# Kernel optimization log

Measured on AMD Instinct MI355X. Metric: run time of the kernel, lower is better.

The kernel has to match this reference:

```python
import jax, jax.numpy as jnp
import numpy as np

S, B, F, D, DF, NH, FH = 1152, 2, 128, 1024, 2048, 8, 4
SEP = 1024
EPS = 1e-5

def ln(x, g, b):
    m = x.mean(-1, keepdims=True)
    v = ((x - m) ** 2).mean(-1, keepdims=True)
    return (x - m) * jax.lax.rsqrt(v + EPS) * g + b

def mha(q, k, v, wi, bi, wo, bo, nh):
    # torch MultiheadAttention, batch_first=False: inputs (L, N, E)
    E = q.shape[-1]
    hd = E // nh
    qh = (q @ wi[:E].T + bi[:E]).reshape(q.shape[0], -1, nh, hd)
    kh = (k @ wi[E:2 * E].T + bi[E:2 * E]).reshape(k.shape[0], -1, nh, hd)
    vh = (v @ wi[2 * E:].T + bi[2 * E:]).reshape(k.shape[0], -1, nh, hd)
    s = jnp.einsum('qnhd,knhd->nhqk', qh, kh) / jnp.sqrt(jnp.float32(hd))
    a = jax.nn.softmax(s, axis=-1)
    o = jnp.einsum('nhqk,knhd->qnhd', a, vh).reshape(q.shape[0], -1, E)
    return o @ wo.T + bo

def setup_inputs() -> dict:
    key = jax.random.key(0)
    it = iter(jax.random.split(key, 40))
    def p(shape, s=0.02):
        return jax.random.normal(next(it), shape, jnp.float32) * s
    z = lambda *sh: jnp.zeros(sh, jnp.float32)
    o = lambda *sh: jnp.ones(sh, jnp.float32)
    return dict(
        src=jax.random.normal(next(it), (S, B, F), jnp.float32),
        sep=SEP,
        sa_wi=p((3 * D, D)), sa_bi=z(3 * D), sa_wo=p((D, D)), sa_bo=z(D),
        fa_wi=p((3 * F, F)), fa_bi=z(3 * F), fa_wo=p((F, F)), fa_bo=z(F),
        pl1_w=p((F, 1)), pl1_b=z(F),
        pl2_w=p((DF, F)), pl2_b=z(DF),
        pl3_w=p((1, DF)), pl3_b=z(1),
        pl4_w=p((DF, F)), pl4_b=z(DF),
        pl5_w=p((D, DF)), pl5_b=z(D),
        pl6_w=p((DF, D)), pl6_b=z(DF),
        pl7_w=p((D, DF)), pl7_b=z(D),
        l1_w=p((DF, D)), l1_b=z(DF),
        l2_w=p((F, DF)), l2_b=z(F),
        pn1_g=o(F), pn1_b=z(F),
        pn2_g=o(D), pn2_b=z(D),
        n1_g=o(D), n1_b=z(D),
        n2_g=o(F), n2_b=z(F),
    )

def _forward(src, sa_wi, sa_bi, sa_wo, sa_bo, fa_wi, fa_bi, fa_wo, fa_bo,
             pl1_w, pl1_b, pl2_w, pl2_b, pl3_w, pl3_b, pl4_w, pl4_b,
             pl5_w, pl5_b, pl6_w, pl6_b, pl7_w, pl7_b, l1_w, l1_b, l2_w, l2_b,
             pn1_g, pn1_b, pn2_g, pn2_b, n1_g, n1_b, n2_g, n2_b, sep):
    Sn, Bn, Fn = src.shape
    relu = jax.nn.relu
    # feature-wise attention: 'b h w -> w (b h) 1'
    x = jnp.transpose(src, (2, 0, 1)).reshape(Fn, Sn * Bn, 1)
    x = x @ pl1_w.T + pl1_b                       # (F, S*B, emsize_f)
    x = mha(x, x, x, fa_wi, fa_bi, fa_wo, fa_bo, FH)
    x = relu(x @ pl2_w.T + pl2_b) @ pl3_w.T + pl3_b  # (F, S*B, 1)
    x = jnp.transpose(x.reshape(Fn, Sn, Bn), (1, 2, 0))  # 'w (b h) 1 -> b h w'
    src1 = ln(x + src, pn1_g, pn1_b)              # (S, B, F)
    src1_ = relu(src1 @ pl4_w.T + pl4_b) @ pl5_w.T + pl5_b  # (S, B, D)
    li = src1_[:sep]
    sl = mha(li, li, li, sa_wi, sa_bi, sa_wo, sa_bo, NH)
    sl = ln(sl + li, pn2_g, pn2_b)
    sl_ = relu(sl @ pl6_w.T + pl6_b) @ pl7_w.T + pl7_b
    sl_ = ln(sl_, pn2_g, pn2_b) + sl
    sr = mha(src1_[sep:], sl_, sl_, sa_wi, sa_bi, sa_wo, sa_bo, NH)
    src2 = jnp.concatenate([sl, sr], axis=0)      # (S, B, D)
    so = ln(src2 + src1_, n1_g, n1_b)
    ff = relu(so @ l1_w.T + l1_b) @ l2_w.T + l2_b  # (S, B, F)
    return ln(src1 + ff, n2_g, n2_b)

def reference(src, sa_wi, sa_bi, sa_wo, sa_bo, fa_wi, fa_bi, fa_wo, fa_bo,
              pl1_w, pl1_b, pl2_w, pl2_b, pl3_w, pl3_b, pl4_w, pl4_b,
              pl5_w, pl5_b, pl6_w, pl6_b, pl7_w, pl7_b, l1_w, l1_b, l2_w, l2_b,
              pn1_g, pn1_b, pn2_g, pn2_b, n1_g, n1_b, n2_g, n2_b, sep):
    return _forward(src, sa_wi, sa_bi, sa_wo, sa_bo, fa_wi, fa_bi, fa_wo, fa_bo,
                    pl1_w, pl1_b, pl2_w, pl2_b, pl3_w, pl3_b, pl4_w, pl4_b,
                    pl5_w, pl5_b, pl6_w, pl6_b, pl7_w, pl7_b, l1_w, l1_b,
                    l2_w, l2_b, pn1_g, pn1_b, pn2_g, pn2_b, n1_g, n1_b,
                    n2_g, n2_b, sep)
```

## Files before the change

kernel.cpp:

```cpp
#include <hip/hip_runtime.h>

using s16x8 = __attribute__((ext_vector_type(8))) short;
using f32x4 = __attribute__((ext_vector_type(4))) float;
using f32x2 = __attribute__((ext_vector_type(2))) float;
typedef unsigned short ushort_t;

__device__ __forceinline__ unsigned short f2bf(float f) {
    union { float f; unsigned u; } v; v.f = f;
    unsigned u = v.u + 0x7FFFu + ((v.u >> 16) & 1u);
    return (unsigned short)(u >> 16);
}
__device__ __forceinline__ float bf2f(unsigned short h) {
    union { unsigned u; float f; } v; v.u = ((unsigned)h) << 16;
    return v.f;
}

__device__ __forceinline__ float block_reduce(float v, int op, float* lds) {
    const int lane = threadIdx.x & 63;
    const int w    = threadIdx.x >> 6;
    const int nw   = blockDim.x >> 6;
#pragma unroll
    for (int off = 32; off > 0; off >>= 1) {
        float o = __shfl_down(v, off, 64);
        v = op ? fmaxf(v, o) : (v + o);
    }
    __syncthreads();
    if (lane == 0) lds[w] = v;
    __syncthreads();
    float r = lds[0];
    for (int i = 1; i < nw; i++) r = op ? fmaxf(r, lds[i]) : (r + lds[i]);
    return r;
}

__device__ __forceinline__ void load_lds16(const void* g, void* l) {
    __builtin_amdgcn_global_load_lds(
        (const __attribute__((address_space(1))) unsigned int*)g,
        (__attribute__((address_space(3))) unsigned int*)l, 16, 0, 0);
}

struct CvtArgs { const float* src[8]; ushort_t* dst[8]; int end[8]; };

__global__ __launch_bounds__(256)
void cvt_all(CvtArgs a)
{
    int i = blockIdx.x * 256 + threadIdx.x;
    int j = 0;
    while (j < 8 && i >= a.end[j]) j++;
    if (j >= 8) return;
    int li = i - (j ? a.end[j - 1] : 0);
    float4 v = *(const float4*)&a.src[j][(size_t)li * 4];
    ushort_t u[4] = { f2bf(v.x), f2bf(v.y), f2bf(v.z), f2bf(v.w) };
    *(uint2*)&a.dst[j][(size_t)li * 4] = *(uint2*)u;
}

template<bool RELU, bool SPLITK>
__global__ __launch_bounds__(256, 2)
void gemm_bf16(const ushort_t* __restrict__ A, const ushort_t* __restrict__ B,
               const float* __restrict__ bias, ushort_t* __restrict__ C,
               float* __restrict__ Cp, long pstride, int ksplen, int zmod,
               int M, int N, int K, int lda, int ldb, int ldc,
               long sAz, long sBz, long sCz, long sA2, long sB2, long sC2,
               int zshift, float alpha)
{
    __shared__ ushort_t As[128 * 32];
    __shared__ ushort_t Bs[128 * 32];

    const int tid = threadIdx.x;
    int zz = blockIdx.z;
    int ks = 0, z = zz;
    if (SPLITK) { ks = zz / zmod; z = zz - ks * zmod; }
    const int z1  = z & ((1 << zshift) - 1);
    const int z2  = z >> zshift;
    const int m0  = blockIdx.x * 128;
    const int n0  = blockIdx.y * 128;

    const ushort_t* Ab = A + (size_t)z1 * sAz + (size_t)z2 * sA2 + (size_t)m0 * lda;
    const ushort_t* Bb = B + (size_t)z1 * sBz + (size_t)z2 * sB2 + (size_t)n0 * ldb;

    const int wave = tid >> 6, lane = tid & 63;
    const int wm = (wave & 1) * 64, wn = (wave >> 1) * 64;
    const int mi = lane & 15, quad = lane >> 4;

    f32x4 acc[4][4];
#pragma unroll
    for (int i = 0; i < 4; i++)
#pragma unroll
        for (int j = 0; j < 4; j++) acc[i][j] = (f32x4)0.f;

    const int r_0 = tid >> 2,           g_0 = (tid & 3) ^ ((r_0 >> 1) & 3);
    const int r_1 = (tid + 256) >> 2,   g_1 = (tid & 3) ^ ((r_1 >> 1) & 3);

    const int kbeg = SPLITK ? ks * ksplen : 0;
    const int kend = SPLITK ? kbeg + ksplen : K;

    for (int k0 = kbeg; k0 < kend; k0 += 32) {
        load_lds16(Ab + (size_t)r_0 * lda + k0 + g_0 * 8, &As[tid * 8]);
        load_lds16(Ab + (size_t)r_1 * lda + k0 + g_1 * 8, &As[(tid + 256) * 8]);
        load_lds16(Bb + (size_t)r_0 * ldb + k0 + g_0 * 8, &Bs[tid * 8]);
        load_lds16(Bb + (size_t)r_1 * ldb + k0 + g_1 * 8, &Bs[(tid + 256) * 8]);
        __syncthreads();

        s16x8 af[4], bfr[4];
#pragma unroll
        for (int t = 0; t < 4; t++) {
            int r = wm + t * 16 + mi;
            af[t] = *(const s16x8*)&As[r * 32 + ((quad ^ ((r >> 1) & 3)) * 8)];
        }
#pragma unroll
        for (int t = 0; t < 4; t++) {
            int r = wn + t * 16 + mi;
            bfr[t] = *(const s16x8*)&Bs[r * 32 + ((quad ^ ((r >> 1) & 3)) * 8)];
        }
#pragma unroll
        for (int tm = 0; tm < 4; tm++)
#pragma unroll
            for (int tn = 0; tn < 4; tn++)
                acc[tm][tn] = __builtin_amdgcn_mfma_f32_16x16x32_bf16(af[tm], bfr[tn], acc[tm][tn], 0, 0, 0);
        __syncthreads();
    }

    if (SPLITK) {
        float* Cf = Cp + (size_t)ks * pstride + (size_t)z1 * sCz + (size_t)z2 * sC2;
#pragma unroll
        for (int tn = 0; tn < 4; tn++) {
            int col = n0 + wn + tn * 16 + mi;
#pragma unroll
            for (int tm = 0; tm < 4; tm++)
#pragma unroll
                for (int r = 0; r < 4; r++) {
                    int row = m0 + wm + tm * 16 + quad * 4 + r;
                    Cf[(size_t)row * ldc + col] = acc[tm][tn][r] * alpha;
                }
        }
    } else {
#pragma unroll
        for (int tn = 0; tn < 4; tn++) {
            int col = n0 + wn + tn * 16 + mi;
            float bv = bias ? bias[col] : 0.f;
#pragma unroll
            for (int tm = 0; tm < 4; tm++) {
#pragma unroll
                for (int r = 0; r < 4; r++) {
                    int row = m0 + wm + tm * 16 + quad * 4 + r;
                    float v = acc[tm][tn][r] * alpha + bv;
                    if (RELU) v = fmaxf(v, 0.f);
                    C[(size_t)z1 * sCz + (size_t)z2 * sC2 + (size_t)row * ldc + col] = f2bf(v);
                }
            }
        }
    }
}

template<bool RELU>
__global__ __launch_bounds__(256)
void sum_cvt(const float* __restrict__ parts, long pstride, int P,
             const float* __restrict__ bias, int ldc,
             ushort_t* __restrict__ out, int total4)
{
    int i = blockIdx.x * 256 + threadIdx.x;
    if (i >= total4) return;
    size_t idx = (size_t)i * 4;
    float4 s = *(const float4*)&parts[idx];
    for (int p = 1; p < P; p++) {
        float4 v = *(const float4*)&parts[(size_t)p * pstride + idx];
        s.x += v.x; s.y += v.y; s.z += v.z; s.w += v.w;
    }
    if (bias) {
        int col = (int)(idx % (size_t)ldc);
        s.x += bias[col]; s.y += bias[col + 1]; s.z += bias[col + 2]; s.w += bias[col + 3];
    }
    if (RELU) {
        s.x = fmaxf(s.x, 0.f); s.y = fmaxf(s.y, 0.f);
        s.z = fmaxf(s.z, 0.f); s.w = fmaxf(s.w, 0.f);
    }
    ushort_t u[4] = { f2bf(s.x), f2bf(s.y), f2bf(s.z), f2bf(s.w) };
    *(uint2*)&out[idx] = *(uint2*)u;
}

__global__ __launch_bounds__(128)
void ln_part(const float* __restrict__ parts, long pstride, int P,
             const float* __restrict__ bias, const ushort_t* __restrict__ resid,
             const float* __restrict__ g, const float* __restrict__ beta,
             float* __restrict__ out)
{
    __shared__ float red[4];
    const int r = blockIdx.x, c = threadIdx.x;
    float x = bias[c] + bf2f(resid[r * 128 + c]);
    for (int p = 0; p < P; p++) x += parts[(size_t)p * pstride + (size_t)r * 128 + c];
    float s  = block_reduce(x, 0, red);
    float ss = block_reduce(x * x, 0, red);
    float mean = s * (1.f / 128.f);
    float var  = ss * (1.f / 128.f) - mean * mean;
    float inv  = rsqrtf(var + 1e-5f);
    out[(size_t)r * 128 + c] = (x - mean) * inv * g[c] + beta[c];
}

__global__ __launch_bounds__(256)
void transp128(const ushort_t* __restrict__ in, ushort_t* __restrict__ out,
               int ldin, long inz1, long inz2, long outz)
{
    __shared__ ushort_t T[64][136];
    const int z = blockIdx.z, z1 = z & 7, z2 = z >> 3;
    const int n0 = blockIdx.x * 64;
    const ushort_t* ip = in + (size_t)z1 * inz1 + (size_t)z2 * inz2;
    const int rr = threadIdx.x >> 2, cg = (threadIdx.x & 3) * 32;
#pragma unroll
    for (int c = 0; c < 4; c++) {
        s16x8 v = *(const s16x8*)(ip + (size_t)(n0 + rr) * ldin + cg + c * 8);
        *(s16x8*)&T[rr][cg + c * 8] = v;
    }
    __syncthreads();
    const int d = threadIdx.x >> 1, j0 = (threadIdx.x & 1) * 32;
    ushort_t* op = out + (size_t)z * outz + (size_t)d * 1024 + n0 + j0;
#pragma unroll
    for (int c = 0; c < 4; c++) {
        s16x8 v;
#pragma unroll
        for (int j = 0; j < 8; j++) v[j] = (short)T[j0 + c * 8 + j][d];
        *(s16x8*)(op + c * 8) = v;
    }
}

__global__ void precomp1(const float* __restrict__ fa_wi, const float* __restrict__ fa_bi,
                         const float* __restrict__ pl1_w, const float* __restrict__ pl1_b,
                         float* __restrict__ consts)
{
    int j = threadIdx.x;
    if (j < 384) {
        float u = 0.f, v = 0.f;
        for (int k = 0; k < 128; k++) {
            float w = fa_wi[j * 128 + k];
            u = fmaf(w, pl1_w[k], u);
            v = fmaf(w, pl1_b[k], v);
        }
        consts[j]       = u;
        consts[512 + j] = v + fa_bi[j];
    }
}

__global__ void precomp2(const float* __restrict__ fa_wo, const float* __restrict__ fa_bo,
                         float* __restrict__ consts)
{
    int tid = threadIdx.x;
    const float* u = consts;
    const float* v = consts + 512;
    if (tid < 16) {
        int h = tid >> 2, w = tid & 3;
        const float* ql = (w < 2) ? u : v;
        const float* kr = ((w & 1) == 0) ? u : v;
        float acc = 0.f;
        for (int d = 0; d < 32; d++) acc += ql[h * 32 + d] * kr[128 + h * 32 + d];
        consts[1024 + tid] = acc * 0.17677669529663687f;
    }
#pragma unroll
    for (int h = 0; h < 4; h++) {
        float acc = 0.f;
        for (int d = 0; d < 32; d++)
            acc = fmaf(fa_wo[tid * 128 + h * 32 + d], u[256 + h * 32 + d], acc);
        consts[1088 + h * 128 + tid] = acc;
    }
    float c0 = fa_bo[tid];
    for (int idx = 0; idx < 128; idx++)
        c0 = fmaf(fa_wo[tid * 128 + idx], v[256 + idx], c0);
    consts[1600 + tid] = c0;
}

__global__ void precomp3(const float* __restrict__ pl2_w, const float* __restrict__ pl2_b,
                         const float* __restrict__ consts, ushort_t* __restrict__ Gb)
{
    int m = blockIdx.x * 256 + threadIdx.x;
    const float* wv = consts + 1088;
    const float* c0 = consts + 1600;
    float a0 = 0.f, ah[4] = {0.f, 0.f, 0.f, 0.f};
    for (int j = 0; j < 128; j++) {
        float w = pl2_w[m * 128 + j];
        ah[0] = fmaf(w, wv[0 * 128 + j], ah[0]);
        ah[1] = fmaf(w, wv[1 * 128 + j], ah[1]);
        ah[2] = fmaf(w, wv[2 * 128 + j], ah[2]);
        ah[3] = fmaf(w, wv[3 * 128 + j], ah[3]);
        a0    = fmaf(w, c0[j], a0);
    }
    ushort_t row[8];
#pragma unroll
    for (int h = 0; h < 4; h++) row[h] = f2bf(ah[h]);
    row[4] = f2bf(a0 + pl2_b[m]);
    row[5] = row[6] = row[7] = 0;
    *(uint4*)&Gb[m * 8] = *(uint4*)row;
}

__global__ __launch_bounds__(512, 6)
void feat_mlp_ln(const float* __restrict__ src, const float* __restrict__ consts,
                 const ushort_t* __restrict__ Gb, const float* __restrict__ pl3_w,
                 const float* __restrict__ pl3_b, const float* __restrict__ pn1_g,
                 const float* __restrict__ pn1_b, ushort_t* __restrict__ src1)
{
    __shared__ ushort_t Gs[2048 * 8];
    __shared__ float    wlds[2048];
    __shared__ ushort_t Ts[128 * 8];
    __shared__ float    sv[128];
    __shared__ float    ypart[4][128];
    __shared__ float    red[8];

    const int n   = blockIdx.x;
    const int tid = threadIdx.x;
    const int f   = tid & 127;
    const int h   = tid >> 7;
    const bool act = (tid < 128);

#pragma unroll
    for (int p = 0; p < 4; p++) {
        int ci = tid + p * 512;
        load_lds16(Gb + (size_t)ci * 8, &Gs[ci * 8]);
    }
    load_lds16(pl3_w + tid * 4, &wlds[tid * 4]);
    if (act) sv[f] = src[n * 128 + f];
    __syncthreads();

    const float si = sv[f];
    float S1 = block_reduce(act ? si : 0.f, 0, red);
    float S2 = block_reduce(act ? si * si : 0.f, 0, red);
    float S3 = block_reduce(act ? si * si * si : 0.f, 0, red);
    float S4 = block_reduce(act ? si * si * si * si : 0.f, 0, red);
    float amax = block_reduce(act ? fabsf(si) : 0.f, 1, red);

    const float p_ = consts[1024 + h * 4 + 0] * si + consts[1024 + h * 4 + 2];
    float pmax = block_reduce(fabsf(p_), 1, red);

    float tt;
    if (pmax * amax < 0.25f) {
        float num = fmaf(p_, fmaf(p_, fmaf(p_, S4 * (1.f / 6.f), 0.5f * S3), S2), S1);
        float den = fmaf(p_, fmaf(p_, fmaf(p_, S3 * (1.f / 6.f), 0.5f * S2), S1), 128.f);
        tt = num / den;
    } else {
        float smax = block_reduce(act ? si : -3.4e38f, 1, red);
        float smin = -block_reduce(act ? -si : -3.4e38f, 1, red);
        float m = fmaxf(p_ * smax, p_ * smin);
        float l = 0.f, t = 0.f;
        for (int j = 0; j < 128; j++) {
            float e = __expf(fmaf(p_, sv[j], -m));
            l += e; t = fmaf(e, sv[j], t);
        }
        tt = t / l;
    }

    Ts[f * 8 + h] = f2bf(tt);
    if (act) {
        Ts[f * 8 + 4] = 0x3F80;
        Ts[f * 8 + 5] = 0; Ts[f * 8 + 6] = 0; Ts[f * 8 + 7] = 0;
    }
    __syncthreads();

    const int wave = tid >> 6, lane = tid & 63;
    const int wm = (wave & 1) * 64;
    const int mq = wave >> 1;
    const int mi = lane & 15, quad = lane >> 4;

    s16x8 af[4];
#pragma unroll
    for (int t = 0; t < 4; t++) {
        s16x8 v = *(const s16x8*)&Ts[(wm + t * 16 + mi) * 8];
        af[t] = (quad == 0) ? v : (s16x8)0;
    }

    f32x2 partial2[4][2];
#pragma unroll
    for (int i = 0; i < 4; i++) { partial2[i][0] = (f32x2)0.f; partial2[i][1] = (f32x2)0.f; }
    const f32x2 zero2 = (f32x2)0.f;

#pragma unroll 4
    for (int mt = 0; mt < 32; mt++) {
        const int m0 = mq * 512 + mt * 16;
        s16x8 bfr = *(const s16x8*)&Gs[(m0 + mi) * 8];
        float w = wlds[m0 + mi];
        f32x2 w2 = { w, w };
        f32x4 acc[4];
#pragma unroll
        for (int tm = 0; tm < 4; tm++)
            acc[tm] = __builtin_amdgcn_mfma_f32_16x16x32_bf16(af[tm], bfr, (f32x4)0.f, 0, 0, 0);
#pragma unroll
        for (int tm = 0; tm < 4; tm++) {
            f32x2* pa = (f32x2*)&acc[tm];
#pragma unroll
            for (int i = 0; i < 2; i++) {
                f32x2 r = __builtin_elementwise_max(pa[i], zero2);
                partial2[tm][i] = r * w2 + partial2[tm][i];
            }
        }
    }

#pragma unroll
    for (int tm = 0; tm < 4; tm++)
#pragma unroll
        for (int r = 0; r < 4; r++) {
            float v = partial2[tm][r >> 1][r & 1];
            v += __shfl_xor(v, 8);
            v += __shfl_xor(v, 4);
            v += __shfl_xor(v, 2);
            v += __shfl_xor(v, 1);
            if (mi == 0) ypart[mq][wm + tm * 16 + quad * 4 + r] = v;
        }
    __syncthreads();

    float yv = 0.f;
    if (act)
        yv = ypart[0][f] + ypart[1][f] + ypart[2][f] + ypart[3][f] + pl3_b[0] + sv[f];
    float s  = block_reduce(yv, 0, red);
    float ss = block_reduce(yv * yv, 0, red);
    float mean = s * (1.f / 128.f);
    float var  = ss * (1.f / 128.f) - mean * mean;
    float inv  = rsqrtf(var + 1e-5f);
    if (act)
        src1[n * 128 + f] = f2bf((yv - mean) * inv * pn1_g[f] + pn1_b[f]);
}

template<bool OUTF32>
__global__ void ln_bf16(const ushort_t* __restrict__ a, const ushort_t* __restrict__ b,
                        const ushort_t* __restrict__ post, const float* __restrict__ g,
                        const float* __restrict__ beta, void* __restrict__ out, int D)
{
    __shared__ float red[4];
    const size_t row = blockIdx.x;
    const int tid = threadIdx.x;
    const int nit = D / blockDim.x;
    const ushort_t* ap = a + row * D;
    const ushort_t* bp = b ? b + row * D : nullptr;
    float xr[4];
    float s = 0.f, ss = 0.f;
    for (int i = 0; i < nit; i++) {
        int idx = i * blockDim.x + tid;
        float x = bf2f(ap[idx]) + (bp ? bf2f(bp[idx]) : 0.f);
        xr[i] = x; s += x; ss = fmaf(x, x, ss);
    }
    s  = block_reduce(s, 0, red);
    ss = block_reduce(ss, 0, red);
    float mean = s / D, var = ss / D - mean * mean;
    float inv = rsqrtf(var + 1e-5f);
    const ushort_t* pp = post ? post + row * D : nullptr;
    for (int i = 0; i < nit; i++) {
        int idx = i * blockDim.x + tid;
        float v = (xr[i] - mean) * inv * g[idx] + beta[idx];
        if (pp) v += bf2f(pp[idx]);
        if (OUTF32) ((float*)out)[row * D + idx] = v;
        else        ((ushort_t*)out)[row * D + idx] = f2bf(v);
    }
}

__global__ void ln_cat(const ushort_t* __restrict__ a1, const ushort_t* __restrict__ a2,
                       int split, const ushort_t* __restrict__ b,
                       const float* __restrict__ g, const float* __restrict__ beta,
                       ushort_t* __restrict__ out, int D)
{
    __shared__ float red[4];
    const int row = blockIdx.x;
    const int tid = threadIdx.x;
    const int nit = D / blockDim.x;
    const ushort_t* ap = (row < split) ? a1 + (size_t)row * D : a2 + (size_t)(row - split) * D;
    const ushort_t* bp = b + (size_t)row * D;
    float xr[4];
    float s = 0.f, ss = 0.f;
    for (int i = 0; i < nit; i++) {
        int idx = i * blockDim.x + tid;
        float x = bf2f(ap[idx]) + bf2f(bp[idx]);
        xr[i] = x; s += x; ss = fmaf(x, x, ss);
    }
    s  = block_reduce(s, 0, red);
    ss = block_reduce(ss, 0, red);
    float mean = s / D, var = ss / D - mean * mean;
    float inv = rsqrtf(var + 1e-5f);
    for (int i = 0; i < nit; i++) {
        int idx = i * blockDim.x + tid;
        out[(size_t)row * D + idx] = f2bf((xr[i] - mean) * inv * g[idx] + beta[idx]);
    }
}

__global__ __launch_bounds__(256)
void softmax_bf16(ushort_t* __restrict__ S)
{
    __shared__ float red[4];
    const size_t row = blockIdx.x;
    ushort_t* p = S + row * 1024;
    const int tid = threadIdx.x;
    uint2 u = *(const uint2*)&p[tid * 4];
    ushort_t* us = (ushort_t*)&u;
    float xr[4];
    float mx = -3.4e38f;
#pragma unroll
    for (int i = 0; i < 4; i++) { xr[i] = bf2f(us[i]); mx = fmaxf(mx, xr[i]); }
    mx = block_reduce(mx, 1, red);
    float sum = 0.f;
#pragma unroll
    for (int i = 0; i < 4; i++) { xr[i] = __expf(xr[i] - mx); sum += xr[i]; }
    sum = block_reduce(sum, 0, red);
    float inv = 1.f / sum;
#pragma unroll
    for (int i = 0; i < 4; i++) us[i] = f2bf(xr[i] * inv);
    *(uint2*)&p[tid * 4] = u;
}

static inline void gemm_go(hipStream_t s, const ushort_t* A, const ushort_t* B,
                           const float* bias, ushort_t* C,
                           int M, int N, int K, int lda, int ldb, int ldc,
                           long sAz, long sBz, long sCz, int Z, float alpha,
                           bool relu,
                           long sA2 = 0, long sB2 = 0, long sC2 = 0, int zshift = 0,
                           int ksplit = 1, float* Cp = nullptr, long pstride = 0)
{
    dim3 g(M / 128, N / 128, Z * ksplit), b(256);
    int ksplen = K / ksplit;
    if (ksplit > 1)
        gemm_bf16<false, true ><<<g, b, 0, s>>>(A, B, nullptr, nullptr, Cp, pstride, ksplen, Z,
            M, N, K, lda, ldb, ldc, sAz, sBz, sCz, sA2, sB2, sC2, zshift, alpha);
    else if (relu)
        gemm_bf16<true,  false><<<g, b, 0, s>>>(A, B, bias, C, nullptr, 0, 0, Z,
            M, N, K, lda, ldb, ldc, sAz, sBz, sCz, sA2, sB2, sC2, zshift, alpha);
    else
        gemm_bf16<false, false><<<g, b, 0, s>>>(A, B, bias, C, nullptr, 0, 0, Z,
            M, N, K, lda, ldb, ldc, sAz, sBz, sCz, sA2, sB2, sC2, zshift, alpha);
}

extern "C" void kernel_launch(void* const* d_in, const int* in_sizes, int n_in,
                              void* d_out, int out_size, void* d_ws, size_t ws_size,
                              hipStream_t stream)
{
    const float* src   = (const float*)d_in[0];
    const float* sa_wi = (const float*)d_in[2];
    const float* sa_bi = (const float*)d_in[3];
    const float* sa_wo = (const float*)d_in[4];
    const float* sa_bo = (const float*)d_in[5];
    const float* fa_wi = (const float*)d_in[6];
    const float* fa_bi = (const float*)d_in[7];
    const float* fa_wo = (const float*)d_in[8];
    const float* fa_bo = (const float*)d_in[9];
    const float* pl1_w = (const float*)d_in[10];
    const float* pl1_b = (const float*)d_in[11];
    const float* pl2_w = (const float*)d_in[12];
    const float* pl2_b = (const float*)d_in[13];
    const float* pl3_w = (const float*)d_in[14];
    const float* pl3_b = (const float*)d_in[15];
    const float* pl4_w = (const float*)d_in[16];
    const float* pl4_b = (const float*)d_in[17];
    const float* pl5_w = (const float*)d_in[18];
    const float* pl5_b = (const float*)d_in[19];
    const float* pl6_w = (const float*)d_in[20];
    const float* pl6_b = (const float*)d_in[21];
    const float* pl7_w = (const float*)d_in[22];
    const float* pl7_b = (const float*)d_in[23];
    const float* l1_w  = (const float*)d_in[24];
    const float* l1_b  = (const float*)d_in[25];
    const float* l2_w  = (const float*)d_in[26];
    const float* l2_b  = (const float*)d_in[27];
    const float* pn1_g = (const float*)d_in[28];
    const float* pn1_b = (const float*)d_in[29];
    const float* pn2_g = (const float*)d_in[30];
    const float* pn2_b = (const float*)d_in[31];
    const float* n1_g  = (const float*)d_in[32];
    const float* n1_b  = (const float*)d_in[33];
    const float* n2_g  = (const float*)d_in[34];
    const float* n2_b  = (const float*)d_in[35];

    float* ws  = (float*)d_ws;
    float* out = (float*)d_out;

    float* CONSTS = ws;
    ushort_t* wsb = (ushort_t*)(ws + 16384);
    ushort_t* SAWIb  = wsb + 0;
    ushort_t* SAWOb  = wsb + 3145728;
    ushort_t* PL4b   = wsb + 4194304;
    ushort_t* PL5b   = wsb + 4456448;
    ushort_t* PL6b   = wsb + 6553600;
    ushort_t* PL7b   = wsb + 8650752;
    ushort_t* L1b    = wsb + 10747904;
    ushort_t* L2b    = wsb + 12845056;
    ushort_t* Gbb    = wsb + 13107200;
    ushort_t* SRC1b  = wsb + 13172736;
    ushort_t* HBIGb  = wsb + 13467648;
    ushort_t* SRC1_b = wsb + 18186240;
    ushort_t* QKVb   = wsb + 20545536;
    ushort_t* SBUFb  = wsb + 27623424;
    ushort_t* OBUFb  = wsb + 44400640;
    ushort_t* SLb    = wsb + 46497792;
    ushort_t* SLPb   = wsb + 48594944;
    ushort_t* SOb    = wsb + 50692096;
    float* PARTS = (float*)SBUFb;

    {
        CvtArgs a;
        const float* srcs[8] = { sa_wi, sa_wo, pl4_w, pl5_w, pl6_w, pl7_w, l1_w, l2_w };
        ushort_t*    dsts[8] = { SAWIb, SAWOb, PL4b, PL5b, PL6b, PL7b, L1b, L2b };
        int          ns[8]   = { 3145728, 1048576, 262144, 2097152, 2097152, 2097152, 2097152, 262144 };
        int cum = 0;
        for (int i = 0; i < 8; i++) { a.src[i] = srcs[i]; a.dst[i] = dsts[i]; cum += ns[i] / 4; a.end[i] = cum; }
        cvt_all<<<(cum + 255) / 256, 256, 0, stream>>>(a);
    }

    precomp1<<<1, 384, 0, stream>>>(fa_wi, fa_bi, pl1_w, pl1_b, CONSTS);
    precomp2<<<1, 128, 0, stream>>>(fa_wo, fa_bo, CONSTS);
    precomp3<<<8, 256, 0, stream>>>(pl2_w, pl2_b, CONSTS, Gbb);
    feat_mlp_ln<<<2304, 512, 0, stream>>>(src, CONSTS, Gbb, pl3_w, pl3_b, pn1_g, pn1_b, SRC1b);

    gemm_go(stream, SRC1b, PL4b, pl4_b, HBIGb, 2304, 2048, 128, 128, 128, 2048, 0, 0, 0, 1, 1.f, true);
    gemm_go(stream, HBIGb, PL5b, nullptr, nullptr, 2304, 1024, 2048, 2048, 2048, 1024, 0, 0, 0, 1, 1.f, false,
            0, 0, 0, 0, 2, PARTS, 2359296);
    sum_cvt<false><<<2304, 256, 0, stream>>>(PARTS, 2359296, 2, pl5_b, 1024, SRC1_b, 589824);

    gemm_go(stream, SRC1_b, SAWIb, sa_bi, QKVb, 2304, 3072, 1024, 1024, 1024, 3072, 0, 0, 0, 1, 1.f, false);
    const float iscale = 0.08838834764831845f;
    ushort_t* VT1 = HBIGb;
    transp128<<<dim3(16, 1, 16), 256, 0, stream>>>(QKVb + 2048, VT1, 6144, 128, 3072, 131072);
    gemm_go(stream, QKVb, QKVb + 1024, nullptr, SBUFb,
            1024, 1024, 128, 6144, 6144, 1024, 128, 128, 1048576, 16, iscale, false,
            3072, 3072, 8388608, 3);
    softmax_bf16<<<16384, 256, 0, stream>>>(SBUFb);
    gemm_go(stream, SBUFb, VT1, nullptr, OBUFb,
            1024, 128, 1024, 1024, 1024, 2048, 1048576, 131072, 128, 16, 1.f, false,
            8388608, 1048576, 1024, 3);
    gemm_go(stream, OBUFb, SAWOb, nullptr, nullptr, 2048, 1024, 1024, 1024, 1024, 1024, 0, 0, 0, 1, 1.f, false,
            0, 0, 0, 0, 2, PARTS, 2097152);
    sum_cvt<false><<<2048, 256, 0, stream>>>(PARTS, 2097152, 2, sa_bo, 1024, HBIGb, 524288);
    ln_bf16<false><<<2048, 256, 0, stream>>>(HBIGb, SRC1_b, nullptr, pn2_g, pn2_b, SLb, 1024);

    gemm_go(stream, SLb, PL6b, nullptr, nullptr, 2048, 2048, 1024, 1024, 1024, 2048, 0, 0, 0, 1, 1.f, false,
            0, 0, 0, 0, 2, PARTS, 4194304);
    sum_cvt<true><<<4096, 256, 0, stream>>>(PARTS, 4194304, 2, pl6_b, 2048, HBIGb, 1048576);
    gemm_go(stream, HBIGb, PL7b, nullptr, nullptr, 2048, 1024, 2048, 2048, 2048, 1024, 0, 0, 0, 1, 1.f, false,
            0, 0, 0, 0, 2, PARTS, 2097152);
    sum_cvt<false><<<2048, 256, 0, stream>>>(PARTS, 2097152, 2, pl7_b, 1024, OBUFb, 524288);
    ln_bf16<false><<<2048, 256, 0, stream>>>(OBUFb, nullptr, SLb, pn2_g, pn2_b, SLPb, 1024);

    ushort_t* KV2 = SBUFb;
    ushort_t* S2  = SBUFb + 4456448;
    ushort_t* SR  = SBUFb + 6553600;
    gemm_go(stream, SLPb, SAWIb + 1024 * 1024, sa_bi + 1024, KV2, 2048, 2048, 1024, 1024, 1024, 2048, 0, 0, 0, 1, 1.f, false);
    ushort_t* VT2 = HBIGb;
    transp128<<<dim3(16, 1, 16), 256, 0, stream>>>(KV2 + 1024, VT2, 4096, 128, 2048, 131072);
    gemm_go(stream, QKVb + 2048 * 3072, KV2, nullptr, S2,
            128, 1024, 128, 6144, 4096, 1024, 128, 128, 131072, 16, iscale, false,
            3072, 2048, 1048576, 3);
    softmax_bf16<<<2048, 256, 0, stream>>>(S2);
    gemm_go(stream, S2, VT2, nullptr, nullptr,
            128, 128, 1024, 1024, 1024, 2048, 131072, 131072, 128, 16, 1.f, false,
            1048576, 1048576, 1024, 3, 8, PARTS, 262144);
    sum_cvt<false><<<256, 256, 0, stream>>>(PARTS, 262144, 8, nullptr, 2048, OBUFb, 65536);
    gemm_go(stream, OBUFb, SAWOb, nullptr, nullptr, 256, 1024, 1024, 1024, 1024, 1024, 0, 0, 0, 1, 1.f, false,
            0, 0, 0, 0, 8, PARTS, 262144);
    sum_cvt<false><<<256, 256, 0, stream>>>(PARTS, 262144, 8, sa_bo, 1024, SR, 65536);

    ln_cat<<<2304, 256, 0, stream>>>(SLb, SR, 2048, SRC1_b, n1_g, n1_b, SOb, 1024);

    gemm_go(stream, SOb, L1b, nullptr, nullptr, 2304, 2048, 1024, 1024, 1024, 2048, 0, 0, 0, 1, 1.f, false,
            0, 0, 0, 0, 2, PARTS, 4718592);
    sum_cvt<true><<<4608, 256, 0, stream>>>(PARTS, 4718592, 2, l1_b, 2048, HBIGb, 1179648);
    gemm_go(stream, HBIGb, L2b, nullptr, nullptr, 2304, 128, 2048, 2048, 2048, 128, 0, 0, 0, 1, 1.f, false,
            0, 0, 0, 0, 8, PARTS, 294912);
    ln_part<<<2304, 128, 0, stream>>>(PARTS, 294912, 8, l2_b, SRC1b, n2_g, n2_b, out);
}
```

Baseline: 589.0 us.

## Split feature attention from MLP+LayerNorm into two kernels via global buffer

The fused feat_mlp_ln kernel is split in two. feat_t uses 128-thread blocks to compute the per-feature attention output for all four heads and writes it to a global bf16 buffer. mlp_ln then loads that buffer straight into MFMA fragments and reuses shared memory for the partial sums. The aim is to cut the many block reductions done by 512 threads and lower shared-memory use so the MLP kernel gets better occupancy, at the cost of an extra launch and a global round trip for the intermediate.

```diff
diff --git a/kernel.cpp b/kernel.cpp
--- a/kernel.cpp
+++ b/kernel.cpp
@@ -288,24 +288,71 @@
     *(uint4*)&Gb[m * 8] = *(uint4*)row;
 }
 
-__global__ __launch_bounds__(512, 6)
-void feat_mlp_ln(const float* __restrict__ src, const float* __restrict__ consts,
-                 const ushort_t* __restrict__ Gb, const float* __restrict__ pl3_w,
-                 const float* __restrict__ pl3_b, const float* __restrict__ pn1_g,
-                 const float* __restrict__ pn1_b, ushort_t* __restrict__ src1)
-{
-    __shared__ ushort_t Gs[2048 * 8];
-    __shared__ float    wlds[2048];
-    __shared__ ushort_t Ts[128 * 8];
-    __shared__ float    sv[128];
-    __shared__ float    ypart[4][128];
-    __shared__ float    red[8];
+__global__ __launch_bounds__(128)
+void feat_t(const float* __restrict__ src, const float* __restrict__ consts,
+            ushort_t* __restrict__ Tp)
+{
+    __shared__ float sv[128];
+    __shared__ float red[2];
+    const int n = blockIdx.x, f = threadIdx.x;
+    const float si = src[n * 128 + f];
+    sv[f] = si;
+    __syncthreads();
+
+    float S1 = block_reduce(si, 0, red);
+    float S2 = block_reduce(si * si, 0, red);
+    float S3 = block_reduce(si * si * si, 0, red);
+    float S4 = block_reduce(si * si * si * si, 0, red);
+    float amax = block_reduce(fabsf(si), 1, red);
+
+    float ph[4];
+#pragma unroll
+    for (int h = 0; h < 4; h++)
+        ph[h] = consts[1024 + h * 4 + 0] * si + consts[1024 + h * 4 + 2];
+    float pm = fmaxf(fmaxf(fabsf(ph[0]), fabsf(ph[1])), fmaxf(fabsf(ph[2]), fabsf(ph[3])));
+    float pmax = block_reduce(pm, 1, red);
+
+    ushort_t row[8];
+    if (pmax * amax < 0.25f) {
+#pragma unroll
+        for (int h = 0; h < 4; h++) {
+            float p = ph[h];
+            float num = fmaf(p, fmaf(p, fmaf(p, S4 * (1.f / 6.f), 0.5f * S3), S2), S1);
+            float den = fmaf(p, fmaf(p, fmaf(p, S3 * (1.f / 6.f), 0.5f * S2), S1), 128.f);
+            row[h] = f2bf(num / den);
+        }
+    } else {
+        float smax = block_reduce(si, 1, red);
+        float smin = -block_reduce(-si, 1, red);
+#pragma unroll
+        for (int h = 0; h < 4; h++) {
+            float p = ph[h];
+            float m = fmaxf(p * smax, p * smin);
+            float l = 0.f, t = 0.f;
+            for (int j = 0; j < 128; j++) {
+                float e = __expf(fmaf(p, sv[j], -m));
+                l += e; t = fmaf(e, sv[j], t);
+            }
+            row[h] = f2bf(t / l);
+        }
+    }
+    row[4] = 0x3F80;
+    row[5] = row[6] = row[7] = 0;
+    *(uint4*)&Tp[(size_t)(n * 128 + f) * 8] = *(uint4*)row;
+}
+
+__global__ __launch_bounds__(512)
+void mlp_ln(const ushort_t* __restrict__ Tp, const float* __restrict__ src,
+            const ushort_t* __restrict__ Gb, const float* __restrict__ pl3_w,
+            const float* __restrict__ pl3_b, const float* __restrict__ pn1_g,
+            const float* __restrict__ pn1_b, ushort_t* __restrict__ src1)
+{
+    __shared__ __align__(16) char smem[40960];
+    ushort_t* Gs   = (ushort_t*)smem;
+    float*    wlds = (float*)(smem + 32768);
 
     const int n   = blockIdx.x;
     const int tid = threadIdx.x;
-    const int f   = tid & 127;
-    const int h   = tid >> 7;
-    const bool act = (tid < 128);
 
 #pragma unroll
     for (int p = 0; p < 4; p++) {
@@ -313,41 +360,6 @@
         load_lds16(Gb + (size_t)ci * 8, &Gs[ci * 8]);
     }
     load_lds16(pl3_w + tid * 4, &wlds[tid * 4]);
-    if (act) sv[f] = src[n * 128 + f];
-    __syncthreads();
-
-    const float si = sv[f];
-    float S1 = block_reduce(act ? si : 0.f, 0, red);
-    float S2 = block_reduce(act ? si * si : 0.f, 0, red);
-    float S3 = block_reduce(act ? si * si * si : 0.f, 0, red);
-    float S4 = block_reduce(act ? si * si * si * si : 0.f, 0, red);
-    float amax = block_reduce(act ? fabsf(si) : 0.f, 1, red);
-
-    const float p_ = consts[1024 + h * 4 + 0] * si + consts[1024 + h * 4 + 2];
-    float pmax = block_reduce(fabsf(p_), 1, red);
-
-    float tt;
-    if (pmax * amax < 0.25f) {
-        float num = fmaf(p_, fmaf(p_, fmaf(p_, S4 * (1.f / 6.f), 0.5f * S3), S2), S1);
-        float den = fmaf(p_, fmaf(p_, fmaf(p_, S3 * (1.f / 6.f), 0.5f * S2), S1), 128.f);
-        tt = num / den;
-    } else {
-        float smax = block_reduce(act ? si : -3.4e38f, 1, red);
-        float smin = -block_reduce(act ? -si : -3.4e38f, 1, red);
-        float m = fmaxf(p_ * smax, p_ * smin);
-        float l = 0.f, t = 0.f;
-        for (int j = 0; j < 128; j++) {
-            float e = __expf(fmaf(p_, sv[j], -m));
-            l += e; t = fmaf(e, sv[j], t);
-        }
-        tt = t / l;
-    }
-
-    Ts[f * 8 + h] = f2bf(tt);
-    if (act) {
-        Ts[f * 8 + 4] = 0x3F80;
-        Ts[f * 8 + 5] = 0; Ts[f * 8 + 6] = 0; Ts[f * 8 + 7] = 0;
-    }
     __syncthreads();
 
     const int wave = tid >> 6, lane = tid & 63;
@@ -358,7 +370,7 @@
     s16x8 af[4];
 #pragma unroll
     for (int t = 0; t < 4; t++) {
-        s16x8 v = *(const s16x8*)&Ts[(wm + t * 16 + mi) * 8];
+        s16x8 v = *(const s16x8*)&Tp[((size_t)n * 128 + wm + t * 16 + mi) * 8];
         af[t] = (quad == 0) ? v : (s16x8)0;
     }
 
@@ -388,6 +400,10 @@
         }
     }
 
+    __syncthreads();
+    float* ypart = (float*)smem;
+    float* red   = (float*)(smem + 4096);
+
 #pragma unroll
     for (int tm = 0; tm < 4; tm++)
 #pragma unroll
@@ -397,19 +413,21 @@
             v += __shfl_xor(v, 4);
             v += __shfl_xor(v, 2);
             v += __shfl_xor(v, 1);
-            if (mi == 0) ypart[mq][wm + tm * 16 + quad * 4 + r] = v;
+            if (mi == 0) ypart[mq * 128 + wm + tm * 16 + quad * 4 + r] = v;
         }
     __syncthreads();
 
     float yv = 0.f;
-    if (act)
-        yv = ypart[0][f] + ypart[1][f] + ypart[2][f] + ypart[3][f] + pl3_b[0] + sv[f];
+    const int f = tid & 127;
+    if (tid < 128)
+        yv = ypart[f] + ypart[128 + f] + ypart[256 + f] + ypart[384 + f]
+           + pl3_b[0] + src[n * 128 + f];
     float s  = block_reduce(yv, 0, red);
     float ss = block_reduce(yv * yv, 0, red);
     float mean = s * (1.f / 128.f);
     float var  = ss * (1.f / 128.f) - mean * mean;
     float inv  = rsqrtf(var + 1e-5f);
-    if (act)
+    if (tid < 128)
         src1[n * 128 + f] = f2bf((yv - mean) * inv * pn1_g[f] + pn1_b[f]);
 }
 
@@ -581,6 +599,7 @@
     ushort_t* SLb    = wsb + 46497792;
     ushort_t* SLPb   = wsb + 48594944;
     ushort_t* SOb    = wsb + 50692096;
+    ushort_t* TPb    = wsb + 53051392;
     float* PARTS = (float*)SBUFb;
 
     {
@@ -596,7 +615,8 @@
     precomp1<<<1, 384, 0, stream>>>(fa_wi, fa_bi, pl1_w, pl1_b, CONSTS);
     precomp2<<<1, 128, 0, stream>>>(fa_wo, fa_bo, CONSTS);
     precomp3<<<8, 256, 0, stream>>>(pl2_w, pl2_b, CONSTS, Gbb);
-    feat_mlp_ln<<<2304, 512, 0, stream>>>(src, CONSTS, Gbb, pl3_w, pl3_b, pn1_g, pn1_b, SRC1b);
+    feat_t<<<2304, 128, 0, stream>>>(src, CONSTS, TPb);
+    mlp_ln<<<2304, 512, 0, stream>>>(TPb, src, Gbb, pl3_w, pl3_b, pn1_g, pn1_b, SRC1b);
 
     gemm_go(stream, SRC1b, PL4b, pl4_b, HBIGb, 2304, 2048, 128, 128, 128, 2048, 0, 0, 0, 1, 1.f, true);
     gemm_go(stream, HBIGb, PL5b, nullptr, nullptr, 2304, 1024, 2048, 2048, 2048, 1024, 0, 0, 0, 1, 1.f, false,
```

New measurement: 589.1 us. About the same (+0.0%).
